# Performance work log

Measured on AMD Instinct MI355X. Metric: run time of the kernel, lower is better.

The kernel has to match this reference:

```python
import jax, jax.numpy as jnp
import numpy as np

EPS = 1e-6

def setup_inputs() -> dict:
    key = jax.random.key(0)
    kq, kk, kv = jax.random.split(key, 3)
    B, H, S, D = 4, 16, 2048, 64
    q = jax.random.normal(kq, (B, H, S, D), dtype=jnp.float32)
    k = jax.random.normal(kk, (B, H, S, D), dtype=jnp.float32)
    v = jax.random.normal(kv, (B, H, S, D), dtype=jnp.float32)
    return {"q": q, "k": k, "v": v}

def reference(q, k, v):
    # ReBASED parallel attention: squared QK^T scores, causal mask, sum-normalized.
    scale = q.shape[-1] ** (-0.5)
    q = q * scale
    # attn: [B, H, S, S]
    attn = jnp.einsum('bhqd,bhkd->bhqk', q, k)
    attn = attn * attn  # squared scores
    S = q.shape[-2]
    causal = jnp.tril(jnp.ones((S, S), dtype=bool))
    attn = jnp.where(causal, attn, 0.0)
    o = jnp.einsum('bhqk,bhkd->bhqd', attn, v)
    z = attn.sum(-1, keepdims=True)
    return o / (z + EPS)
```

## Files before the change

### kernel.cpp

```cpp
#include <hip/hip_runtime.h>
#include <hip/hip_bf16.h>


#define SEQ 2048
#define HD  64
#define BQ  128
#define BK  64

typedef __attribute__((ext_vector_type(8))) short bf16x8;
typedef __attribute__((ext_vector_type(4))) short bf16x4;
typedef __attribute__((ext_vector_type(4))) float f32x4;
typedef __attribute__((ext_vector_type(4))) unsigned u32x4;

__device__ inline unsigned packbf(float a, float b) {
    __hip_bfloat162 h = __float22bfloat162_rn(make_float2(a, b));
    union { __hip_bfloat162 h2; unsigned u; } cv; cv.h2 = h; return cv.u;
}

__device__ inline void gload_lds16(const void* g, void* l) {
    __builtin_amdgcn_global_load_lds(
        (const __attribute__((address_space(1))) unsigned*)g,
        (__attribute__((address_space(3))) unsigned*)l, 16, 0, 0);
}

__global__ __launch_bounds__(256)
void convert_kv_kernel(const float* __restrict__ kg, const float* __restrict__ vg,
                       unsigned short* __restrict__ kws, unsigned short* __restrict__ vws) {
    const int head = blockIdx.x;
    const int kt   = blockIdx.y;
    const int t    = threadIdx.x;
    const size_t gbase = (size_t)head * SEQ * HD + (size_t)kt * BK * HD;
    unsigned short* ktile = kws + gbase;
    unsigned short* vtile = vws + gbase;

    {
        const int r = t >> 2, qr = t & 3;
        #pragma unroll
        for (int gg = 0; gg < 2; ++gg) {
            const int g = qr * 2 + gg;
            float4 a = *(const float4*)(kg + gbase + r * HD + g * 8);
            float4 b = *(const float4*)(kg + gbase + r * HD + g * 8 + 4);
            u32x4 pkd;
            pkd[0] = packbf(a.x, a.y); pkd[1] = packbf(a.z, a.w);
            pkd[2] = packbf(b.x, b.y); pkd[3] = packbf(b.z, b.w);
            *(u32x4*)(ktile + r * 64 + ((g ^ (r & 7)) << 3)) = pkd;
        }
    }
    {
        const int d = t & 63, sg0 = t >> 6;
        #pragma unroll
        for (int i = 0; i < 4; ++i) {
            const int sg = sg0 + i * 4;
            float v0 = vg[gbase + (sg * 4 + 0) * HD + d];
            float v1 = vg[gbase + (sg * 4 + 1) * HD + d];
            float v2 = vg[gbase + (sg * 4 + 2) * HD + d];
            float v3 = vg[gbase + (sg * 4 + 3) * HD + d];
            uint2 pkd = make_uint2(packbf(v0, v1), packbf(v2, v3));
            *(uint2*)(vtile + d * 64 + ((sg ^ (d & 15)) << 2)) = pkd;
        }
    }
}

__global__ __launch_bounds__(256, 4)
void rebased_r9_kernel(const float* __restrict__ qg,
                       const unsigned short* __restrict__ kws,
                       const unsigned short* __restrict__ vws,
                       float* __restrict__ og) {
    __shared__ __align__(16) unsigned short Ks[2][BK][HD];
    __shared__ __align__(16) unsigned short Vst[2][HD][BK];

    const int t    = threadIdx.x;
    const int lane = t & 63;
    const int w    = t >> 6;
    const int li   = lane & 15;
    const int qd   = lane >> 4;
    const int head = blockIdx.x;
    const int qt   = 15 - blockIdx.y;
    const int ktmax = 2 * qt + 1;
    const size_t base = (size_t)head * SEQ * HD;

    bf16x8 qf[2][2];
    {
        const int qrow0 = qt * BQ + w * 32;
        #pragma unroll
        for (int mt = 0; mt < 2; ++mt) {
            const float* qrow = qg + base + (size_t)(qrow0 + mt * 16 + li) * HD;
            #pragma unroll
            for (int ks = 0; ks < 2; ++ks) {
                float4 a = *(const float4*)(qrow + ks * 32 + qd * 8);
                float4 b = *(const float4*)(qrow + ks * 32 + qd * 8 + 4);
                union { unsigned u[4]; bf16x8 v; } cv;
                cv.u[0] = packbf(a.x * 0.125f, a.y * 0.125f);
                cv.u[1] = packbf(a.z * 0.125f, a.w * 0.125f);
                cv.u[2] = packbf(b.x * 0.125f, b.y * 0.125f);
                cv.u[3] = packbf(b.z * 0.125f, b.w * 0.125f);
                qf[ks][mt] = cv.v;
            }
        }
    }

    const int woff = w * 1024;
    const int goff = woff + lane * 16;
    #define STAGE(b, kt2)                                                          \
    {                                                                              \
        const char* ksrc = (const char*)(kws + base + (size_t)(kt2) * BK * HD);    \
        const char* vsrc = (const char*)(vws + base + (size_t)(kt2) * BK * HD);    \
        char* kdst = (char*)&Ks[b][0][0];                                          \
        char* vdst = (char*)&Vst[b][0][0];                                         \
        gload_lds16(ksrc + goff,        kdst + woff);                              \
        gload_lds16(ksrc + goff + 4096, kdst + woff + 4096);                       \
        gload_lds16(vsrc + goff,        vdst + woff);                              \
        gload_lds16(vsrc + goff + 4096, vdst + woff + 4096);                       \
    }

    #define WAITBAR4 asm volatile("s_waitcnt vmcnt(4)\n\ts_barrier" ::: "memory")
    #define WAITBAR0 asm volatile("s_waitcnt vmcnt(0)\n\ts_barrier" ::: "memory")
    #define ENDBAR   asm volatile("s_waitcnt lgkmcnt(0)\n\ts_barrier" ::: "memory")

    f32x4 oacc[2][4];
    f32x4 zacc[2];
    #pragma unroll
    for (int mt = 0; mt < 2; ++mt) {
        zacc[mt] = (f32x4){0.f, 0.f, 0.f, 0.f};
        #pragma unroll
        for (int nd = 0; nd < 4; ++nd) oacc[mt][nd] = (f32x4){0.f, 0.f, 0.f, 0.f};
    }
    bf16x4 onesb;
    { union { unsigned short us[4]; bf16x4 v; } o;
      o.us[0] = o.us[1] = o.us[2] = o.us[3] = 0x3F80; onesb = o.v; }

    const int qrow_min = qt * BQ + w * 32;

    #define COMPUTE(curq, ktq)                                                         \
    {                                                                                  \
        const bool active = ((ktq) * BK <= qrow_min + 31);                             \
        if (active) {                                                                  \
            const bool needmask = ((ktq) * BK + 63 > qrow_min);                        \
            _Pragma("unroll")                                                          \
            for (int h = 0; h < 2; ++h) {                                              \
                f32x4 stt[2][2];                                                       \
                _Pragma("unroll")                                                      \
                for (int n2 = 0; n2 < 2; ++n2)                                         \
                    _Pragma("unroll")                                                  \
                    for (int mt = 0; mt < 2; ++mt)                                     \
                        stt[n2][mt] = (f32x4){0.f, 0.f, 0.f, 0.f};                     \
                _Pragma("unroll")                                                      \
                for (int ks = 0; ks < 2; ++ks) {                                       \
                    bf16x8 kf[2];                                                      \
                    _Pragma("unroll")                                                  \
                    for (int n2 = 0; n2 < 2; ++n2) {                                   \
                        const int row = (h * 2 + n2) * 16 + li;                        \
                        const int grp = ((ks * 4 + qd) ^ (li & 7)) << 3;               \
                        kf[n2] = *(const bf16x8*)&Ks[curq][row][grp];                  \
                    }                                                                  \
                    _Pragma("unroll")                                                  \
                    for (int n2 = 0; n2 < 2; ++n2)                                     \
                        _Pragma("unroll")                                              \
                        for (int mt = 0; mt < 2; ++mt)                                 \
                            stt[n2][mt] = __builtin_amdgcn_mfma_f32_16x16x32_bf16(     \
                                kf[n2], qf[ks][mt], stt[n2][mt], 0, 0, 0);             \
                }                                                                      \
                unsigned pk[2][2][2];                                                  \
                _Pragma("unroll")                                                      \
                for (int n2 = 0; n2 < 2; ++n2) {                                       \
                    const int kcb = (ktq) * BK + (h * 2 + n2) * 16 + qd * 4;           \
                    _Pragma("unroll")                                                  \
                    for (int mt = 0; mt < 2; ++mt) {                                   \
                        const int qrow = qrow_min + mt * 16 + li;                      \
                        float p[4];                                                    \
                        _Pragma("unroll")                                              \
                        for (int r = 0; r < 4; ++r) {                                  \
                            float s = stt[n2][mt][r];                                  \
                            if (needmask && (kcb + r > qrow)) s = 0.f;                 \
                            p[r] = s * s;                                              \
                        }                                                              \
                        pk[n2][mt][0] = packbf(p[0], p[1]);                            \
                        pk[n2][mt][1] = packbf(p[2], p[3]);                            \
                    }                                                                  \
                }                                                                      \
                _Pragma("unroll")                                                      \
                for (int s2 = 0; s2 < 2; ++s2) {                                       \
                    bf16x4 av[2];                                                      \
                    _Pragma("unroll")                                                  \
                    for (int mt = 0; mt < 2; ++mt) {                                   \
                        union { unsigned u[2]; bf16x4 v; } cv;                         \
                        cv.u[0] = pk[s2][mt][0]; cv.u[1] = pk[s2][mt][1];              \
                        av[mt] = cv.v;                                                 \
                    }                                                                  \
                    _Pragma("unroll")                                                  \
                    for (int mt = 0; mt < 2; ++mt)                                     \
                        zacc[mt] = __builtin_amdgcn_mfma_f32_16x16x16bf16_1k(          \
                            av[mt], onesb, zacc[mt], 0, 0, 0);                         \
                    const int sg = (h * 2 + s2) * 4 + qd;                              \
                    _Pragma("unroll")                                                  \
                    for (int nd = 0; nd < 4; ++nd) {                                   \
                        const int d = nd * 16 + li;                                    \
                        bf16x4 vf = *(const bf16x4*)&Vst[curq][d][(sg ^ li) << 2];     \
                        _Pragma("unroll")                                              \
                        for (int mt = 0; mt < 2; ++mt)                                 \
                            oacc[mt][nd] = __builtin_amdgcn_mfma_f32_16x16x16bf16_1k(  \
                                av[mt], vf, oacc[mt][nd], 0, 0, 0);                    \
                    }                                                                  \
                }                                                                      \
            }                                                                          \
        }                                                                              \
    }

    STAGE(0, 0);

    for (int kt = 0; kt <= ktmax; kt += 2) {
        STAGE(1, kt + 1);
        WAITBAR4;
        COMPUTE(0, kt);
        ENDBAR;

        if (kt + 1 < ktmax) { STAGE(0, kt + 2); WAITBAR4; }
        else                { WAITBAR0; }
        COMPUTE(1, kt + 1);
        if (kt + 1 < ktmax) { ENDBAR; }
    }

    float* odst = og + base + (size_t)qt * BQ * HD;
    #pragma unroll
    for (int mt = 0; mt < 2; ++mt) {
        #pragma unroll
        for (int r = 0; r < 4; ++r) {
            float inv = 1.f / (zacc[mt][r] + 1e-6f);
            int row = w * 32 + mt * 16 + qd * 4 + r;
            #pragma unroll
            for (int nd = 0; nd < 4; ++nd)
                odst[row * HD + nd * 16 + li] = oacc[mt][nd][r] * inv;
        }
    }
}

extern "C" void kernel_launch(void* const* d_in, const int* in_sizes, int n_in,
                              void* d_out, int out_size, void* d_ws, size_t ws_size,
                              hipStream_t stream) {
    const float* q = (const float*)d_in[0];
    const float* k = (const float*)d_in[1];
    const float* v = (const float*)d_in[2];
    float* out = (float*)d_out;

    unsigned short* kws = (unsigned short*)d_ws;
    unsigned short* vws = kws + (size_t)64 * SEQ * HD;

    dim3 cgrid(64, 32);
    convert_kv_kernel<<<cgrid, dim3(256), 0, stream>>>(k, v, kws, vws);

    dim3 grid(64, 16);
    rebased_r9_kernel<<<grid, dim3(256), 0, stream>>>(q, kws, vws, out);
}
```

Baseline: 188.9 us.

## Split long causal query tiles across two blocks with atomic-flag reduction

The eight longest causal query tiles per head have their key range split in half across two blocks. Each half writes partial outputs and normalizers to workspace. An atomic counter picks whichever block finishes last to combine both halves and write the normalized result. This is meant to balance load across the grid and shorten the tail made by the longest tiles, at the cost of extra partial-result traffic, fences and a larger workspace requirement. The split is used only when the workspace is large enough.

Result: slower. 410.7 us (+117.4%).

```diff
diff --git a/kernel.cpp b/kernel.cpp
--- a/kernel.cpp
+++ b/kernel.cpp
@@ -25,13 +25,16 @@
 
 __global__ __launch_bounds__(256)
 void convert_kv_kernel(const float* __restrict__ kg, const float* __restrict__ vg,
-                       unsigned short* __restrict__ kws, unsigned short* __restrict__ vws) {
+                       unsigned short* __restrict__ kws, unsigned short* __restrict__ vws,
+                       int* __restrict__ flags, int dozero) {
     const int head = blockIdx.x;
     const int kt   = blockIdx.y;
     const int t    = threadIdx.x;
     const size_t gbase = (size_t)head * SEQ * HD + (size_t)kt * BK * HD;
     unsigned short* ktile = kws + gbase;
     unsigned short* vtile = vws + gbase;
+
+    if (dozero && kt == 0 && t < 8) flags[(head << 3) | t] = 0;
 
     {
         const int r = t >> 2, qr = t & 3;
@@ -62,12 +65,17 @@
 }
 
 __global__ __launch_bounds__(256, 4)
-void rebased_r9_kernel(const float* __restrict__ qg,
-                       const unsigned short* __restrict__ kws,
-                       const unsigned short* __restrict__ vws,
-                       float* __restrict__ og) {
+void rebased_r11_kernel(const float* __restrict__ qg,
+                        const unsigned short* __restrict__ kws,
+                        const unsigned short* __restrict__ vws,
+                        float* __restrict__ og,
+                        float* __restrict__ opart,
+                        float* __restrict__ zpart,
+                        int* __restrict__ flags,
+                        int nsplit) {
     __shared__ __align__(16) unsigned short Ks[2][BK][HD];
     __shared__ __align__(16) unsigned short Vst[2][HD][BK];
+    __shared__ int sOld;
 
     const int t    = threadIdx.x;
     const int lane = t & 63;
@@ -75,8 +83,13 @@
     const int li   = lane & 15;
     const int qd   = lane >> 4;
     const int head = blockIdx.x;
-    const int qt   = 15 - blockIdx.y;
-    const int ktmax = 2 * qt + 1;
+    const int y    = blockIdx.y;
+
+    int qt, kt0, ktN, part; bool issplit;
+    if (y < nsplit)  { issplit = true;  part = 0; qt = 15 - y; kt0 = 0;      ktN = qt; }
+    else if (y < 16) { issplit = false; part = 0; qt = 15 - y; kt0 = 0;      ktN = 2 * qt + 1; }
+    else             { issplit = true;  part = 1; qt = 31 - y; kt0 = qt + 1; ktN = 2 * qt + 1; }
+    const int niters = ktN - kt0 + 1;
     const size_t base = (size_t)head * SEQ * HD;
 
     bf16x8 qf[2][2];
@@ -206,30 +219,73 @@
         }                                                                              \
     }
 
-    STAGE(0, 0);
-
-    for (int kt = 0; kt <= ktmax; kt += 2) {
-        STAGE(1, kt + 1);
-        WAITBAR4;
-        COMPUTE(0, kt);
+    STAGE(0, kt0);
+    for (int i = 0; ; i += 2) {
+        const int ktA = kt0 + i;
+        const bool haveB = (i + 1 < niters);
+        if (haveB) { STAGE(1, ktA + 1); WAITBAR4; } else { WAITBAR0; }
+        COMPUTE(0, ktA);
+        if (!haveB) break;
         ENDBAR;
 
-        if (kt + 1 < ktmax) { STAGE(0, kt + 2); WAITBAR4; }
-        else                { WAITBAR0; }
-        COMPUTE(1, kt + 1);
-        if (kt + 1 < ktmax) { ENDBAR; }
+        const int ktB = ktA + 1;
+        const bool haveC = (i + 2 < niters);
+        if (haveC) { STAGE(0, ktB + 1); WAITBAR4; } else { WAITBAR0; }
+        COMPUTE(1, ktB);
+        if (!haveC) break;
+        ENDBAR;
     }
 
     float* odst = og + base + (size_t)qt * BQ * HD;
-    #pragma unroll
-    for (int mt = 0; mt < 2; ++mt) {
-        #pragma unroll
-        for (int r = 0; r < 4; ++r) {
-            float inv = 1.f / (zacc[mt][r] + 1e-6f);
-            int row = w * 32 + mt * 16 + qd * 4 + r;
+    if (!issplit) {
+        #pragma unroll
+        for (int mt = 0; mt < 2; ++mt) {
             #pragma unroll
-            for (int nd = 0; nd < 4; ++nd)
-                odst[row * HD + nd * 16 + li] = oacc[mt][nd][r] * inv;
+            for (int r = 0; r < 4; ++r) {
+                float inv = 1.f / (zacc[mt][r] + 1e-6f);
+                int row = w * 32 + mt * 16 + qd * 4 + r;
+                #pragma unroll
+                for (int nd = 0; nd < 4; ++nd)
+                    odst[row * HD + nd * 16 + li] = oacc[mt][nd][r] * inv;
+            }
+        }
+    } else {
+        const int tile = (head << 3) | (qt - 8);
+        float* my_o = part ? (opart + (size_t)tile * BQ * HD) : odst;
+        float* my_z = zpart + ((size_t)tile * 2 + part) * BQ;
+
+        #pragma unroll
+        for (int mt = 0; mt < 2; ++mt) {
+            #pragma unroll
+            for (int r = 0; r < 4; ++r) {
+                int row = w * 32 + mt * 16 + qd * 4 + r;
+                if (li == 0) my_z[row] = zacc[mt][r];
+                #pragma unroll
+                for (int nd = 0; nd < 4; ++nd)
+                    my_o[row * HD + nd * 16 + li] = oacc[mt][nd][r];
+            }
+        }
+
+        __threadfence();
+        __syncthreads();
+        if (t == 0) sOld = atomicAdd(&flags[tile], 1);
+        __syncthreads();
+        if (sOld == 0) return;
+
+        __threadfence();
+        const float* po = part ? odst : (opart + (size_t)tile * BQ * HD);
+        const float* pz = zpart + ((size_t)tile * 2 + (1 - part)) * BQ;
+        #pragma unroll
+        for (int mt = 0; mt < 2; ++mt) {
+            #pragma unroll
+            for (int r = 0; r < 4; ++r) {
+                int row = w * 32 + mt * 16 + qd * 4 + r;
+                float inv = 1.f / (zacc[mt][r] + pz[row] + 1e-6f);
+                #pragma unroll
+                for (int nd = 0; nd < 4; ++nd)
+                    odst[row * HD + nd * 16 + li] =
+                        (oacc[mt][nd][r] + po[row * HD + nd * 16 + li]) * inv;
+            }
         }
     }
 }
@@ -242,12 +298,19 @@
     const float* v = (const float*)d_in[2];
     float* out = (float*)d_out;
 
+    const size_t KVBYTES = (size_t)64 * SEQ * HD * 2;
     unsigned short* kws = (unsigned short*)d_ws;
-    unsigned short* vws = kws + (size_t)64 * SEQ * HD;
+    unsigned short* vws = (unsigned short*)((char*)d_ws + KVBYTES);
+    float* opart = (float*)((char*)d_ws + 2 * KVBYTES);
+    float* zpart = (float*)((char*)opart + (size_t)512 * BQ * HD * 4);
+    int*   flags = (int*)((char*)zpart + (size_t)512 * 2 * BQ * 4);
+    const size_t NEED = ((char*)(flags + 512)) - (char*)d_ws;
+
+    const int nsplit = (ws_size >= NEED) ? 8 : 0;
 
     dim3 cgrid(64, 32);
-    convert_kv_kernel<<<cgrid, dim3(256), 0, stream>>>(k, v, kws, vws);
-
-    dim3 grid(64, 16);
-    rebased_r9_kernel<<<grid, dim3(256), 0, stream>>>(q, kws, vws, out);
-}
+    convert_kv_kernel<<<cgrid, dim3(256), 0, stream>>>(k, v, kws, vws, flags, nsplit ? 1 : 0);
+
+    dim3 grid(64, nsplit ? 24 : 16);
+    rebased_r11_kernel<<<grid, dim3(256), 0, stream>>>(q, kws, vws, out, opart, zpart, flags, nsplit);
+}
```
